# Kernel optimization log

Measured on AMD Instinct MI355X. Metric: run time of the kernel, lower is better.

Reference implementation:

```python
import jax, jax.numpy as jnp
import numpy as np

B_, L, DM = 2, 1024, 1024
DIN = 2048            # expand * d_model
HD = 64               # headdim
NH = DIN // HD        # 32 heads
DS = 64               # d_state
NG = 1                # ngroups
TH = NH * (DS // 2)   # theta dim = 1024
SPLITS = np.cumsum([DIN, DIN, NG * DS, NG * DS, NH, TH]).tolist()
EPS = 1e-5

def _rms(x, w):
    return x * jax.lax.rsqrt(jnp.mean(x * x, -1, keepdims=True) + EPS) * w

def setup_inputs():
    ks = jax.random.split(jax.random.key(0), 8)
    d_in = 2 * DIN + 2 * NG * DS + NH + TH + NH  # 5312
    u = jax.random.normal(ks[0], (B_, L, DM), jnp.float32)
    in_proj_w = jax.random.normal(ks[1], (d_in, DM), jnp.float32) * 0.02
    out_proj_w = jax.random.normal(ks[2], (DM, DIN), jnp.float32) * 0.02
    # dt_bias init as in module: inv-softplus of dt ~ logUniform(dt_min, dt_max)
    dt = jnp.exp(jax.random.uniform(ks[3], (NH,)) * (np.log(0.1) - np.log(0.001)) + np.log(0.001))
    dt_bias = dt + jnp.log(-jnp.expm1(-dt))
    A_log = jnp.log(jax.random.uniform(ks[4], (NH,), minval=1.0, maxval=16.0))
    D = jnp.ones((NH,), jnp.float32)
    B_norm_w = jnp.ones((DS,), jnp.float32)
    C_norm_w = jnp.ones((DS,), jnp.float32)
    B_bias = jnp.ones((NH, DS), jnp.float32)
    C_bias = jnp.ones((NH, DS), jnp.float32)
    norm_w = jnp.ones((DIN,), jnp.float32)
    return dict(u=u, in_proj_w=in_proj_w, dt_bias=dt_bias, A_log=A_log, D=D,
                B_norm_w=B_norm_w, C_norm_w=C_norm_w, B_bias=B_bias, C_bias=C_bias,
                norm_w=norm_w, out_proj_w=out_proj_w)

def reference(u, in_proj_w, dt_bias, A_log, D, B_norm_w, C_norm_w, B_bias, C_bias, norm_w, out_proj_w):
    zxbcdt = u @ in_proj_w.T                                  # (b,l,5312)
    z, x, Br, Cr, dtr, thr, lamr = jnp.split(zxbcdt, SPLITS, axis=-1)
    dt = jax.nn.softplus(dtr + dt_bias)                       # (b,l,h)
    A = -jnp.exp(A_log)                                       # (h,) negative
    x = x.reshape(B_, L, NH, HD)
    # BC norm at group level, then group->head expansion, then head-specific bias
    Bg = _rms(Br.reshape(B_, L, NG, DS), B_norm_w)
    Cg = _rms(Cr.reshape(B_, L, NG, DS), C_norm_w)
    Bh = jnp.broadcast_to(Bg, (B_, L, NH, DS)) + B_bias
    Ch = jnp.broadcast_to(Cg, (B_, L, NH, DS)) + C_bias
    # data-dependent RoPE with cumulative angles
    th_cs = jnp.cumsum(thr.reshape(B_, L, NH, DS // 2), axis=1)
    c, s = jnp.cos(th_cs), jnp.sin(th_cs)
    def rot(v):
        v1, v2 = v[..., :DS // 2], v[..., DS // 2:]
        return jnp.concatenate([v1 * c - v2 * s, v1 * s + v2 * c], -1)
    Bh, Ch = rot(Bh), rot(Ch)
    # trapezoidal discretization coefficients
    lam = jax.nn.sigmoid(lamr)                                # (b,l,h) in [0,1]
    alpha = jnp.exp(dt * A)
    gamma = lam * dt
    beta = (1.0 - lam) * dt * alpha
    def step(carry, inp):
        h, bx_prev = carry
        x_t, B_t, C_t, a_t, b_t, g_t = inp
        bx = x_t[..., :, None] * B_t[..., None, :]            # (b,h,p,n)
        h = a_t[..., None, None] * h + b_t[..., None, None] * bx_prev + g_t[..., None, None] * bx
        y = jnp.einsum('bhn,bhpn->bhp', C_t, h)
        return (h, bx), y
    m = lambda t: jnp.moveaxis(t, 1, 0)                       # seq-major for scan
    h0 = jnp.zeros((B_, NH, HD, DS), u.dtype)
    _, ys = jax.lax.scan(step, (h0, h0), (m(x), m(Bh), m(Ch), m(alpha), m(beta), m(gamma)))
    y = jnp.moveaxis(ys, 0, 1) + x * D[:, None]               # D skip, per head
    y = y.reshape(B_, L, DIN)
    # RMSNormGated, norm_before_gate=False: norm(y * silu(z)) * w
    g = y * jax.nn.silu(z)
    out = _rms(g, norm_w)
    return out @ out_proj_w.T
```

## Files before the change

### kernel.cpp

```cpp
#include <hip/hip_runtime.h>
#include <hip/hip_bf16.h>

#define DMODEL 1024
#define DIN    2048
#define NH     32
#define HD     64
#define DS     64
#define LSEQ   1024
#define BB     2
#define DTOT   5312
#define ROWS   (BB*LSEQ)
#define OFF_Z   0
#define OFF_X   2048
#define OFF_BR  4096
#define OFF_CR  4160
#define OFF_DT  4224
#define OFF_TH  4256
#define OFF_LAM 5280
#define NZX     4096
#define NREM    (DTOT - NZX)
#define NSEG 8
#define SEG  (LSEQ / NSEG)

typedef short  s16x8 __attribute__((ext_vector_type(8)));
typedef float  f32x4 __attribute__((ext_vector_type(4)));
typedef unsigned short u16;

__device__ __forceinline__ unsigned int f2bf(float f) {
    unsigned int u = __float_as_uint(f);
    u += 0x7fffu + ((u >> 16) & 1u);
    return u >> 16;
}
__device__ __forceinline__ unsigned int pk(float x, float y) {
    return f2bf(x) | (f2bf(y) << 16);
}
__device__ __forceinline__ void split1(float v, u16& hi, u16& lo) {
    const unsigned int h = f2bf(v);
    hi = (u16)h;
    lo = (u16)f2bf(v - __uint_as_float(h << 16));
}
__device__ __forceinline__ void split8(const float4 a, const float4 b,
                                       s16x8& hi, s16x8& lo) {
    u16 h_, l_;
    split1(a.x, h_, l_); hi[0] = (short)h_; lo[0] = (short)l_;
    split1(a.y, h_, l_); hi[1] = (short)h_; lo[1] = (short)l_;
    split1(a.z, h_, l_); hi[2] = (short)h_; lo[2] = (short)l_;
    split1(a.w, h_, l_); hi[3] = (short)h_; lo[3] = (short)l_;
    split1(b.x, h_, l_); hi[4] = (short)h_; lo[4] = (short)l_;
    split1(b.y, h_, l_); hi[5] = (short)h_; lo[5] = (short)l_;
    split1(b.z, h_, l_); hi[6] = (short)h_; lo[6] = (short)l_;
    split1(b.w, h_, l_); hi[7] = (short)h_; lo[7] = (short)l_;
}
__device__ __forceinline__ void cvt8(const float4 a, const float4 b, s16x8& hi) {
    hi[0] = (short)f2bf(a.x); hi[1] = (short)f2bf(a.y);
    hi[2] = (short)f2bf(a.z); hi[3] = (short)f2bf(a.w);
    hi[4] = (short)f2bf(b.x); hi[5] = (short)f2bf(b.y);
    hi[6] = (short)f2bf(b.z); hi[7] = (short)f2bf(b.w);
}

typedef const __attribute__((address_space(1))) unsigned int glb_u32;
typedef __attribute__((address_space(3))) unsigned int lds_u32;
__device__ __forceinline__ void gload16(const void* g, void* l) {
    __builtin_amdgcn_global_load_lds((glb_u32*)g, (lds_u32*)l, 16, 0, 0);
}

#define SWZ(row) (((row) >> 1) & 3)

__global__ __launch_bounds__(256) void conv_u(const float* __restrict__ src,
        u16* __restrict__ hi, u16* __restrict__ lo) {
    const size_t i4 = ((size_t)blockIdx.x * 256 + threadIdx.x) * 4;
    const float4 v = *(const float4*)(src + i4);
    const unsigned int h0 = f2bf(v.x), h1 = f2bf(v.y), h2 = f2bf(v.z), h3 = f2bf(v.w);
    uint2 hw, lw;
    hw.x = h0 | (h1 << 16); hw.y = h2 | (h3 << 16);
    lw.x = pk(v.x - __uint_as_float(h0 << 16), v.y - __uint_as_float(h1 << 16));
    lw.y = pk(v.z - __uint_as_float(h2 << 16), v.w - __uint_as_float(h3 << 16));
    *(uint2*)(hi + i4) = hw;
    *(uint2*)(lo + i4) = lw;
}

__global__ __launch_bounds__(256) void conv_w(const float* __restrict__ src,
        u16* __restrict__ hi, u16* __restrict__ lo) {
    const size_t i4 = ((size_t)blockIdx.x * 256 + threadIdx.x) * 4;
    const float4 v = *(const float4*)(src + i4);
    const unsigned int h0 = f2bf(v.x), h1 = f2bf(v.y), h2 = f2bf(v.z), h3 = f2bf(v.w);
    uint2 hw, lw;
    hw.x = h0 | (h1 << 16); hw.y = h2 | (h3 << 16);
    lw.x = pk(v.x - __uint_as_float(h0 << 16), v.y - __uint_as_float(h1 << 16));
    lw.y = pk(v.z - __uint_as_float(h2 << 16), v.w - __uint_as_float(h3 << 16));
    *(uint2*)(hi + i4) = hw;
    if ((i4 >> 10) >= NZX)
        *(uint2*)(lo + (i4 - (size_t)NZX * DMODEL)) = lw;
}

__global__ __launch_bounds__(256) void conv_wo(const float* __restrict__ src,
        u16* __restrict__ hi) {
    const size_t i4 = ((size_t)blockIdx.x * 256 + threadIdx.x) * 4;
    const float4 v = *(const float4*)(src + i4);
    uint2 hw;
    hw.x = pk(v.x, v.y); hw.y = pk(v.z, v.w);
    *(uint2*)(hi + i4) = hw;
}

__global__ __launch_bounds__(256) void mfma_gemm_zx(const u16* __restrict__ uA_,
                                                    const u16* __restrict__ uW,
                                                    float* __restrict__ zx) {
    __shared__ u16 Al[2][128 * 32];
    __shared__ u16 Bl[2][128 * 32];
    const int tid = threadIdx.x;
    const int m0 = blockIdx.y * 128, n0 = blockIdx.x * 128;
    const int lane = tid & 63, wave = tid >> 6;
    const int wr = wave >> 1, wc = wave & 1;
    const int lr = lane >> 4, lc = lane & 15;
    const int sr = tid >> 2;
    const int sc = (((tid & 3) ^ SWZ(tid >> 2)) * 8);

    f32x4 acc[4][4] = {};

    const u16* pA = uA_ + (size_t)(m0 + sr) * DMODEL + sc;
    const u16* pB = uW  + (size_t)(n0 + sr) * DMODEL + sc;

#define STAGE_ZX(buf, k0) {                                              \
        gload16(pA + (k0), &Al[buf][tid * 8]);                           \
        gload16(pA + (k0) + (size_t)64 * DMODEL, &Al[buf][tid * 8 + 2048]); \
        gload16(pB + (k0), &Bl[buf][tid * 8]);                           \
        gload16(pB + (k0) + (size_t)64 * DMODEL, &Bl[buf][tid * 8 + 2048]); }

    STAGE_ZX(0, 0);
    __syncthreads();
    int cur = 0;
    for (int k0 = 0; k0 < DMODEL; k0 += 32) {
        if (k0 + 32 < DMODEL) STAGE_ZX(cur ^ 1, k0 + 32);
        s16x8 af[4], bf[4];
        #pragma unroll
        for (int f = 0; f < 4; ++f) {
            const int ra = wr * 64 + f * 16 + lc;
            af[f] = *(const s16x8*)&Al[cur][ra * 32 + ((lr ^ SWZ(ra)) * 8)];
            const int rb = wc * 64 + f * 16 + lc;
            bf[f] = *(const s16x8*)&Bl[cur][rb * 32 + ((lr ^ SWZ(rb)) * 8)];
        }
        #pragma unroll
        for (int fm = 0; fm < 4; ++fm)
            #pragma unroll
            for (int fn = 0; fn < 4; ++fn)
                acc[fm][fn] = __builtin_amdgcn_mfma_f32_16x16x32_bf16(
                    af[fm], bf[fn], acc[fm][fn], 0, 0, 0);
        __syncthreads();
        cur ^= 1;
    }
#undef STAGE_ZX

    #pragma unroll
    for (int fm = 0; fm < 4; ++fm)
        #pragma unroll
        for (int fn = 0; fn < 4; ++fn) {
            const size_t col = n0 + wc * 64 + fn * 16 + lc;
            #pragma unroll
            for (int j = 0; j < 4; ++j) {
                const size_t row = m0 + wr * 64 + fm * 16 + lr * 4 + j;
                zx[row * DTOT + col] = acc[fm][fn][j];
            }
        }
}

__global__ __launch_bounds__(256) void mfma_gemm_out(const u16* __restrict__ A,
                                                     const u16* __restrict__ B,
                                                     float* __restrict__ C,
                                                     int K, int ldc) {
    __shared__ u16 Als[2][128 * 32];
    __shared__ u16 Bls[2][64 * 32];
    const int tid = threadIdx.x;
    const int m0 = blockIdx.y * 128, n0 = blockIdx.x * 64;
    const int lane = tid & 63, wave = tid >> 6;
    const int wr = wave >> 1, wc = wave & 1;
    const int lr = lane >> 4, lc = lane & 15;
    const int sr = tid >> 2;
    const int sc = (((tid & 3) ^ SWZ(tid >> 2)) * 8);

    f32x4 acc[4][2] = {};

    const u16* pA = A + (size_t)(m0 + sr) * K + sc;
    const u16* pB = B + (size_t)(n0 + sr) * K + sc;

#define STAGE_OUT(buf, k0) {                                             \
        gload16(pA + (k0), &Als[buf][tid * 8]);                          \
        gload16(pA + (k0) + (size_t)64 * K, &Als[buf][tid * 8 + 2048]);  \
        gload16(pB + (k0), &Bls[buf][tid * 8]); }

    STAGE_OUT(0, 0);
    __syncthreads();
    int cur = 0;
    for (int k0 = 0; k0 < K; k0 += 32) {
        if (k0 + 32 < K) STAGE_OUT(cur ^ 1, k0 + 32);
        s16x8 af[4], bf[2];
        #pragma unroll
        for (int f = 0; f < 4; ++f) {
            const int ra = wr * 64 + f * 16 + lc;
            af[f] = *(const s16x8*)&Als[cur][ra * 32 + ((lr ^ SWZ(ra)) * 8)];
        }
        #pragma unroll
        for (int f = 0; f < 2; ++f) {
            const int rb = wc * 32 + f * 16 + lc;
            bf[f] = *(const s16x8*)&Bls[cur][rb * 32 + ((lr ^ SWZ(rb)) * 8)];
        }
        #pragma unroll
        for (int fm = 0; fm < 4; ++fm)
            #pragma unroll
            for (int fn = 0; fn < 2; ++fn)
                acc[fm][fn] = __builtin_amdgcn_mfma_f32_16x16x32_bf16(
                    af[fm], bf[fn], acc[fm][fn], 0, 0, 0);
        __syncthreads();
        cur ^= 1;
    }
#undef STAGE_OUT

    #pragma unroll
    for (int fm = 0; fm < 4; ++fm)
        #pragma unroll
        for (int fn = 0; fn < 2; ++fn) {
            const size_t col = n0 + wc * 32 + fn * 16 + lc;
            #pragma unroll
            for (int j = 0; j < 4; ++j) {
                const size_t row = m0 + wr * 64 + fm * 16 + lr * 4 + j;
                C[row * (size_t)ldc + col] = acc[fm][fn][j];
            }
        }
}

__global__ __launch_bounds__(256) void mfma_gemm_rem3(const u16* __restrict__ uh,
        const u16* __restrict__ ul, const u16* __restrict__ wh,
        const u16* __restrict__ wl, float* __restrict__ zxr) {
    __shared__ u16 Ah[2][128 * 32], Alo[2][128 * 32];
    __shared__ u16 Bh[2][64 * 32],  Blo[2][64 * 32];
    const int tid = threadIdx.x;
    const int m0 = blockIdx.y * 128, n0 = blockIdx.x * 64;
    const int lane = tid & 63, wave = tid >> 6;
    const int wr = wave >> 1, wc = wave & 1;
    const int lr = lane >> 4, lc = lane & 15;
    const int sr = tid >> 2;
    const int sc = (((tid & 3) ^ SWZ(tid >> 2)) * 8);

    f32x4 acc[4][2] = {};

    const u16* pAh = uh + (size_t)(m0 + sr) * DMODEL + sc;
    const u16* pAl = ul + (size_t)(m0 + sr) * DMODEL + sc;
    const u16* pBh = wh + (size_t)(n0 + sr) * DMODEL + sc;
    const u16* pBl = wl + (size_t)(n0 + sr) * DMODEL + sc;

#define STAGE_R3(buf, k0) {                                                  \
        gload16(pAh + (k0), &Ah[buf][tid * 8]);                              \
        gload16(pAh + (k0) + (size_t)64 * DMODEL, &Ah[buf][tid * 8 + 2048]); \
        gload16(pAl + (k0), &Alo[buf][tid * 8]);                             \
        gload16(pAl + (k0) + (size_t)64 * DMODEL, &Alo[buf][tid * 8 + 2048]);\
        gload16(pBh + (k0), &Bh[buf][tid * 8]);                              \
        gload16(pBl + (k0), &Blo[buf][tid * 8]); }

    STAGE_R3(0, 0);
    __syncthreads();
    int cur = 0;
    for (int k0 = 0; k0 < DMODEL; k0 += 32) {
        if (k0 + 32 < DMODEL) STAGE_R3(cur ^ 1, k0 + 32);
        s16x8 ahf[4], alf[4], bhf[2], blf[2];
        #pragma unroll
        for (int f = 0; f < 4; ++f) {
            const int ra = wr * 64 + f * 16 + lc;
            const int oa = ra * 32 + ((lr ^ SWZ(ra)) * 8);
            ahf[f] = *(const s16x8*)&Ah[cur][oa];
            alf[f] = *(const s16x8*)&Alo[cur][oa];
        }
        #pragma unroll
        for (int f = 0; f < 2; ++f) {
            const int rb = wc * 32 + f * 16 + lc;
            const int ob = rb * 32 + ((lr ^ SWZ(rb)) * 8);
            bhf[f] = *(const s16x8*)&Bh[cur][ob];
            blf[f] = *(const s16x8*)&Blo[cur][ob];
        }
        #pragma unroll
        for (int fm = 0; fm < 4; ++fm)
            #pragma unroll
            for (int fn = 0; fn < 2; ++fn) {
                acc[fm][fn] = __builtin_amdgcn_mfma_f32_16x16x32_bf16(
                    ahf[fm], bhf[fn], acc[fm][fn], 0, 0, 0);
                acc[fm][fn] = __builtin_amdgcn_mfma_f32_16x16x32_bf16(
                    ahf[fm], blf[fn], acc[fm][fn], 0, 0, 0);
                acc[fm][fn] = __builtin_amdgcn_mfma_f32_16x16x32_bf16(
                    alf[fm], bhf[fn], acc[fm][fn], 0, 0, 0);
            }
        __syncthreads();
        cur ^= 1;
    }
#undef STAGE_R3

    #pragma unroll
    for (int fm = 0; fm < 4; ++fm)
        #pragma unroll
        for (int fn = 0; fn < 2; ++fn) {
            const size_t col = n0 + wc * 32 + fn * 16 + lc;
            #pragma unroll
            for (int j = 0; j < 4; ++j) {
                const size_t row = m0 + wr * 64 + fm * 16 + lr * 4 + j;
                zxr[row * DTOT + col] = acc[fm][fn][j];
            }
        }
}

__global__ __launch_bounds__(64) void prep_kernel(const float* __restrict__ zx,
        const float* __restrict__ dt_bias, const float* __restrict__ A_log,
        const float* __restrict__ B_norm_w, const float* __restrict__ C_norm_w,
        float* __restrict__ Bg, float* __restrict__ Cg,
        float4* __restrict__ abg4) {
    const int bl = blockIdx.x;
    const int b = bl >> 10, l = bl & (LSEQ - 1);
    const int t  = threadIdx.x;
    const float* row = zx + (size_t)bl * DTOT;
    const float br = row[OFF_BR + t];
    const float cr = row[OFF_CR + t];
    float ssb = br * br, ssc = cr * cr;
    #pragma unroll
    for (int k = 1; k < 64; k <<= 1) { ssb += __shfl_xor(ssb, k); ssc += __shfl_xor(ssc, k); }
    const float scB = rsqrtf(ssb * (1.f / 64.f) + 1e-5f);
    const float scC = rsqrtf(ssc * (1.f / 64.f) + 1e-5f);
    Bg[(size_t)bl * 64 + t] = br * scB * B_norm_w[t];
    Cg[(size_t)bl * 64 + t] = cr * scC * C_norm_w[t];
    if (t < NH) {
        const float dtr = row[OFF_DT + t] + dt_bias[t];
        const float dt  = (dtr > 20.f) ? dtr : log1pf(expf(dtr));
        const float lamr = row[OFF_LAM + t];
        const float lam  = 1.f / (1.f + expf(-lamr));
        const float Ah   = -expf(A_log[t]);
        const float al   = expf(dt * Ah);
        const float bp   = (1.f - lam) * dt;
        const size_t o = ((size_t)b * NH + t) * LSEQ + l;
        abg4[o] = make_float4(al, bp * al, lam * dt, bp);
    }
}

__global__ __launch_bounds__(256) void cumsum_kernel(const float* __restrict__ zx,
                                                     float* __restrict__ th_cs) {
    const int bh = blockIdx.x;
    const int b = bh >> 5, h = bh & 31;
    const int d = threadIdx.x & 31, seg = threadIdx.x >> 5;
    const float* base = zx + (size_t)b * LSEQ * DTOT + OFF_TH + h * 32 + d;
    float* out = th_cs + (size_t)b * LSEQ * 1024 + h * 32 + d;
    __shared__ float sums[8][33];
    const int l0 = seg * 128;
    float s = 0.f;
    #pragma unroll 4
    for (int i = 0; i < 128; ++i) s += base[(size_t)(l0 + i) * DTOT];
    sums[seg][d] = s;
    __syncthreads();
    float acc = 0.f;
    for (int s2 = 0; s2 < seg; ++s2) acc += sums[s2][d];
    #pragma unroll 4
    for (int i = 0; i < 128; ++i) {
        acc += base[(size_t)(l0 + i) * DTOT];
        out[(size_t)(l0 + i) * 1024] = acc;
    }
}

__global__ __launch_bounds__(256) void rot_kernel(const float* __restrict__ th_cs,
        const float* __restrict__ Bg, const float* __restrict__ Cg,
        const float* __restrict__ B_bias, const float* __restrict__ C_bias,
        float* __restrict__ Brot, float* __restrict__ Crot) {
    const size_t idx = (size_t)blockIdx.x * 256 + threadIdx.x;
    const int j = (int)(idx & 31);
    const int h = (int)((idx >> 5) & 31);
    const size_t bl = idx >> 10;
    const int l = (int)(bl & (LSEQ - 1));
    const int b = (int)(bl >> 10);
    const float th = th_cs[idx];
    float s, c;
    sincosf(th, &s, &c);
    float v1 = Bg[bl * 64 + j]      + B_bias[h * 64 + j];
    float v2 = Bg[bl * 64 + 32 + j] + B_bias[h * 64 + 32 + j];
    const size_t ob = ((size_t)(b * NH + h) * LSEQ + l) * DS + j;
    Brot[ob]      = v1 * c - v2 * s;
    Brot[ob + 32] = v1 * s + v2 * c;
    v1 = Cg[bl * 64 + j]      + C_bias[h * 64 + j];
    v2 = Cg[bl * 64 + 32 + j] + C_bias[h * 64 + 32 + j];
    Crot[ob]      = v1 * c - v2 * s;
    Crot[ob + 32] = v1 * s + v2 * c;
}

__global__ __launch_bounds__(64) void wcalc_kernel(const float4* __restrict__ abg4,
        float* __restrict__ wbuf, float* __restrict__ aprod,
        float* __restrict__ bscale, float* __restrict__ Lbuf) {
    const int bh = blockIdx.x;
    const int lane = threadIdx.x;
    const int seg = lane >> 3, sub = lane & 7;
    const int t0 = seg * SEG;
    const int sbase = t0 + sub * 16;
    const float4* ab = abg4 + (size_t)bh * LSEQ;

    float part = 0.f;
    #pragma unroll
    for (int i = 0; i < 16; ++i) part += logf(ab[sbase + i].x);
    float incl = part;
    #pragma unroll
    for (int d = 1; d < 8; d <<= 1) {
        const float v = __shfl_up(incl, d, 8);
        if (sub >= d) incl += v;
    }
    const float LE = __shfl(incl, 7, 8);
    float Lrun = incl - part;

    for (int i = 0; i < 16; ++i) {
        const int s = sbase + i;
        const float4 A = ab[s];
        Lrun += logf(A.x);
        Lbuf[(size_t)bh * LSEQ + s] = Lrun;
        float w;
        if ((s & (SEG - 1)) == (SEG - 1)) w = A.z;
        else w = __expf(LE - Lrun) * (A.z + ab[s + 1].w);
        wbuf[(size_t)bh * LSEQ + s] = w;
    }
    if (sub == 0) {
        aprod[bh * NSEG + seg] = __expf(LE);
        bscale[bh * NSEG + seg] = (seg > 0) ? __expf(LE) * ab[t0].w : 0.f;
    }
}

#define WK 136
__global__ __launch_bounds__(256) void hseg_gemm(const float* __restrict__ zx,
        const float* __restrict__ Brot, const float* __restrict__ wbuf,
        float* __restrict__ hseg) {
    __shared__ u16 XH[64][WK], XL[64][WK], BHs[64][WK], BLs[64][WK];
    const int blk = blockIdx.x;
    const int seg = blk & (NSEG - 1), bh = blk >> 3;
    const int b = bh >> 5, h = bh & 31;
    const int tid = threadIdx.x;

    {
        const int sIdx = tid >> 1, half = tid & 1;
        const int t = seg * SEG + sIdx;
        const float wv = wbuf[(size_t)bh * LSEQ + t];
        const float* xsrc = zx + ((size_t)b * LSEQ + t) * DTOT + OFF_X + h * 64 + half * 32;
        const float* bsrc = Brot + ((size_t)bh * LSEQ + t) * DS + half * 32;
        #pragma unroll
        for (int i = 0; i < 32; i += 4) {
            const float4 xv = *(const float4*)(xsrc + i);
            const float4 bv = *(const float4*)(bsrc + i);
            const int p0 = half * 32 + i;
            u16 hi, lo;
            split1(xv.x * wv, hi, lo); XH[p0 + 0][sIdx] = hi; XL[p0 + 0][sIdx] = lo;
            split1(xv.y * wv, hi, lo); XH[p0 + 1][sIdx] = hi; XL[p0 + 1][sIdx] = lo;
            split1(xv.z * wv, hi, lo); XH[p0 + 2][sIdx] = hi; XL[p0 + 2][sIdx] = lo;
            split1(xv.w * wv, hi, lo); XH[p0 + 3][sIdx] = hi; XL[p0 + 3][sIdx] = lo;
            split1(bv.x, hi, lo); BHs[p0 + 0][sIdx] = hi; BLs[p0 + 0][sIdx] = lo;
            split1(bv.y, hi, lo); BHs[p0 + 1][sIdx] = hi; BLs[p0 + 1][sIdx] = lo;
            split1(bv.z, hi, lo); BHs[p0 + 2][sIdx] = hi; BLs[p0 + 2][sIdx] = lo;
            split1(bv.w, hi, lo); BHs[p0 + 3][sIdx] = hi; BLs[p0 + 3][sIdx] = lo;
        }
    }
    __syncthreads();

    const int lane = tid & 63, wave = tid >> 6;
    const int wR = wave >> 1, wC = wave & 1;
    const int lr = lane >> 4, lc = lane & 15;

    f32x4 acc[2][2] = {};
    #pragma unroll
    for (int ks = 0; ks < 4; ++ks) {
        const int k0 = ks * 32;
        s16x8 xh[2], xl[2], bhf[2], blf[2];
        #pragma unroll
        for (int f = 0; f < 2; ++f) {
            const int pr = wR * 32 + f * 16 + lc;
            xh[f] = *(const s16x8*)&XH[pr][k0 + lr * 8];
            xl[f] = *(const s16x8*)&XL[pr][k0 + lr * 8];
            const int nr = wC * 32 + f * 16 + lc;
            bhf[f] = *(const s16x8*)&BHs[nr][k0 + lr * 8];
            blf[f] = *(const s16x8*)&BLs[nr][k0 + lr * 8];
        }
        #pragma unroll
        for (int fm = 0; fm < 2; ++fm)
            #pragma unroll
            for (int fn = 0; fn < 2; ++fn) {
                acc[fm][fn] = __builtin_amdgcn_mfma_f32_16x16x32_bf16(
                    xh[fm], bhf[fn], acc[fm][fn], 0, 0, 0);
                acc[fm][fn] = __builtin_amdgcn_mfma_f32_16x16x32_bf16(
                    xh[fm], blf[fn], acc[fm][fn], 0, 0, 0);
                acc[fm][fn] = __builtin_amdgcn_mfma_f32_16x16x32_bf16(
                    xl[fm], bhf[fn], acc[fm][fn], 0, 0, 0);
            }
    }

    float* hp = hseg + ((size_t)(bh * NSEG + seg) * HD) * DS;
    #pragma unroll
    for (int fm = 0; fm < 2; ++fm)
        #pragma unroll
        for (int fn = 0; fn < 2; ++fn) {
            const int n = wC * 32 + fn * 16 + lc;
            #pragma unroll
            for (int j = 0; j < 4; ++j) {
                const int p = wR * 32 + fm * 16 + lr * 4 + j;
                hp[p * DS + n] = acc[fm][fn][j];
            }
        }
}

__global__ __launch_bounds__(256) void scan_fix(float* __restrict__ hseg,
        const float* __restrict__ aprod, const float* __restrict__ bscale,
        const float* __restrict__ zx, const float* __restrict__ Brot,
        const float4* __restrict__ abg4) {
    const int blk = blockIdx.x;
    const int ptile = blk & 3, h = (blk >> 2) & 31, b = blk >> 7;
    const int tid = threadIdx.x;
    const int pl = tid >> 4, ng = tid & 15;
    const int p = ptile * 16 + pl;
    const int n0 = ng * 4;
    const size_t bh = (size_t)b * NH + h;

    float4 cur = make_float4(0.f, 0.f, 0.f, 0.f);
    #pragma unroll
    for (int s = 0; s < NSEG; ++s) {
        float* hp = hseg + (((bh * NSEG + s) * HD + p) * DS + n0);
        float4 tmp = *(const float4*)hp;
        float4 hst = cur;
        if (s > 0) {
            const float bs = bscale[bh * NSEG + s];
            const float bp0 = abg4[bh * LSEQ + s * SEG].w;
            const int tm1 = s * SEG - 1;
            const float4 Bm = *(const float4*)(Brot + ((size_t)bh * LSEQ + tm1) * DS + n0);
            const float xm = zx[((size_t)b * LSEQ + tm1) * DTOT + OFF_X + h * HD + p];
            const float fb = bs * xm;
            const float f1 = bp0 * xm;
            tmp.x = fmaf(fb, Bm.x, tmp.x);
            tmp.y = fmaf(fb, Bm.y, tmp.y);
            tmp.z = fmaf(fb, Bm.z, tmp.z);
            tmp.w = fmaf(fb, Bm.w, tmp.w);
            hst.x = fmaf(f1, Bm.x, hst.x);
            hst.y = fmaf(f1, Bm.y, hst.y);
            hst.z = fmaf(f1, Bm.z, hst.z);
            hst.w = fmaf(f1, Bm.w, hst.w);
        }
        *(float4*)hp = hst;
        const float a = aprod[bh * NSEG + s];
        cur.x = fmaf(a, cur.x, tmp.x);
        cur.y = fmaf(a, cur.y, tmp.y);
        cur.z = fmaf(a, cur.z, tmp.z);
        cur.w = fmaf(a, cur.w, tmp.w);
    }
}

#define GWF 132
#define XTS 72
__global__ __launch_bounds__(256, 2) void ssd_y(const float* __restrict__ zx,
        const float* __restrict__ Brot, const float* __restrict__ Crot,
        const float4* __restrict__ abg4, const float* __restrict__ hseg,
        const float* __restrict__ Lbuf, const float* __restrict__ Dp,
        float* __restrict__ yb) {
    __shared__ float Gw[128 * GWF];
    __shared__ u16 XTh[64 * XTS];
    __shared__ float Ls[128], gbs[128], gms[128], eLs[128];

    const int blk = blockIdx.x;
    const int seg = blk & (NSEG - 1), bh = blk >> 3;
    const int b = bh >> 5, h = bh & 31;
    const int tid = threadIdx.x;
    const int t0 = seg * SEG;
    const int lane = tid & 63, wave = tid >> 6;
    const int wr = wave >> 1, wc = wave & 1;
    const int lr = lane >> 4, lc = lane & 15;

    if (tid < 128) {
        const int t = t0 + tid;
        const float4 A = abg4[(size_t)bh * LSEQ + t];
        const float Lv = Lbuf[(size_t)bh * LSEQ + t];
        Ls[tid] = Lv;
        gms[tid] = A.z;
        gbs[tid] = (tid < 127) ? A.z + abg4[(size_t)bh * LSEQ + t + 1].w : 0.f;
        eLs[tid] = __expf(Lv);
    }
    __syncthreads();

    const float* Cbase = Crot + ((size_t)bh * LSEQ + t0) * DS;
    const float* Bbase = Brot + ((size_t)bh * LSEQ + t0) * DS;
    const float* Hbase = hseg + ((size_t)(bh * NSEG + seg) * HD) * DS;
    const float* Xbase = zx + ((size_t)b * LSEQ + t0) * DTOT + OFF_X + h * 64;

    f32x4 accP[4][2] = {};
    f32x4 accG[4][4] = {};
    #pragma unroll
    for (int ks = 0; ks < 2; ++ks) {
        const int k0 = ks * 32 + lr * 8;
        s16x8 ch[4], cl4[4], bh4[4], bl4[4], hh2[2];
        #pragma unroll
        for (int f = 0; f < 4; ++f) {
            const int rowc = wr * 64 + f * 16 + lc;
            const float4 c0 = *(const float4*)(Cbase + (size_t)rowc * DS + k0);
            const float4 c1 = *(const float4*)(Cbase + (size_t)rowc * DS + k0 + 4);
            split8(c0, c1, ch[f], cl4[f]);
            const int rowb = wc * 64 + f * 16 + lc;
            const float4 b0 = *(const float4*)(Bbase + (size_t)rowb * DS + k0);
            const float4 b1 = *(const float4*)(Bbase + (size_t)rowb * DS + k0 + 4);
            split8(b0, b1, bh4[f], bl4[f]);
        }
        #pragma unroll
        for (int f = 0; f < 2; ++f) {
            const int rowp = wc * 32 + f * 16 + lc;
            const float4 h0 = *(const float4*)(Hbase + (size_t)rowp * DS + k0);
            const float4 h1 = *(const float4*)(Hbase + (size_t)rowp * DS + k0 + 4);
            cvt8(h0, h1, hh2[f]);
        }
        #pragma unroll
        for (int fm = 0; fm < 4; ++fm) {
            #pragma unroll
            for (int fn = 0; fn < 4; ++fn) {
                accG[fm][fn] = __builtin_amdgcn_mfma_f32_16x16x32_bf16(
                    ch[fm], bh4[fn], accG[fm][fn], 0, 0, 0);
                accG[fm][fn] = __builtin_amdgcn_mfma_f32_16x16x32_bf16(
                    ch[fm], bl4[fn], accG[fm][fn], 0, 0, 0);
                accG[fm][fn] = __builtin_amdgcn_mfma_f32_16x16x32_bf16(
                    cl4[fm], bh4[fn], accG[fm][fn], 0, 0, 0);
            }
            #pragma unroll
            for (int fn = 0; fn < 2; ++fn) {
                accP[fm][fn] = __builtin_amdgcn_mfma_f32_16x16x32_bf16(
                    ch[fm], hh2[fn], accP[fm][fn], 0, 0, 0);
                accP[fm][fn] = __builtin_amdgcn_mfma_f32_16x16x32_bf16(
                    cl4[fm], hh2[fn], accP[fm][fn], 0, 0, 0);
            }
        }
    }

    const float Dh = Dp[h];
    #pragma unroll
    for (int fm = 0; fm < 4; ++fm)
        #pragma unroll
        for (int fn = 0; fn < 4; ++fn)
            #pragma unroll
            for (int jj = 0; jj < 4; ++jj) {
                const int i = wr * 64 + fm * 16 + lr * 4 + jj;
                const int j = wc * 64 + fn * 16 + lc;
                float v;
                if (j < i)       v = accG[fm][fn][jj] * __expf(Ls[i] - Ls[j]) * gbs[j];
                else if (j == i) v = accG[fm][fn][jj] * gms[i] + Dh;
                else             v = 0.f;
                Gw[i * GWF + j] = v;
            }

    f32x4 accY[4][2];
    #pragma unroll
    for (int fm = 0; fm < 4; ++fm)
        #pragma unroll
        for (int fn = 0; fn < 2; ++fn)
            #pragma unroll
            for (int jj = 0; jj < 4; ++jj) {
                const int i = wr * 64 + fm * 16 + lr * 4 + jj;
                accY[fm][fn][jj] = eLs[i] * accP[fm][fn][jj];
            }

#define STAGE_XT(H) {                                                        \
        const int lp = tid >> 2, pq = (tid & 3) * 16;                        \
        const float* xs = Xbase + (size_t)((H) * 64 + lp) * DTOT + pq;       \
        _Pragma("unroll")                                                    \
        for (int i = 0; i < 16; i += 4) {                                    \
            const float4 xv = *(const float4*)(xs + i);                      \
            XTh[(pq + i + 0) * XTS + lp] = (u16)f2bf(xv.x);                  \
            XTh[(pq + i + 1) * XTS + lp] = (u16)f2bf(xv.y);                  \
            XTh[(pq + i + 2) * XTS + lp] = (u16)f2bf(xv.z);                  \
            XTh[(pq + i + 3) * XTS + lp] = (u16)f2bf(xv.w);                  \
        }                                                                    \
    }
    STAGE_XT(0);
    __syncthreads();

    #pragma unroll
    for (int ks = 0; ks < 4; ++ks) {
        if (ks == 2) {
            __syncthreads();
            STAGE_XT(1);
            __syncthreads();
        }
        const int k0 = ks * 32 + lr * 8;
        const int kl = (ks & 1) * 32 + lr * 8;
        s16x8 gh4[4], gl4[4], xf[2];
        #pragma unroll
        for (int f = 0; f < 4; ++f) {
            const int rowi = wr * 64 + f * 16 + lc;
            const float4 g0 = *(const float4*)&Gw[rowi * GWF + k0];
            const float4 g1 = *(const float4*)&Gw[rowi * GWF + k0 + 4];
            split8(g0, g1, gh4[f], gl4[f]);
        }
        #pragma unroll
        for (int f = 0; f < 2; ++f) {
            const int rowp = wc * 32 + f * 16 + lc;
            xf[f] = *(const s16x8*)&XTh[rowp * XTS + kl];
        }
        #pragma unroll
        for (int fm = 0; fm < 4; ++fm)
            #pragma unroll
            for (int fn = 0; fn < 2; ++fn) {
                accY[fm][fn] = __builtin_amdgcn_mfma_f32_16x16x32_bf16(
                    gh4[fm], xf[fn], accY[fm][fn], 0, 0, 0);
                accY[fm][fn] = __builtin_amdgcn_mfma_f32_16x16x32_bf16(
                    gl4[fm], xf[fn], accY[fm][fn], 0, 0, 0);
            }
    }
#undef STAGE_XT

    #pragma unroll
    for (int fm = 0; fm < 4; ++fm)
        #pragma unroll
        for (int fn = 0; fn < 2; ++fn) {
            const int p = wc * 32 + fn * 16 + lc;
            #pragma unroll
            for (int jj = 0; jj < 4; ++jj) {
                const int i = wr * 64 + fm * 16 + lr * 4 + jj;
                yb[((size_t)b * LSEQ + t0 + i) * DIN + h * 64 + p] = accY[fm][fn][jj];
            }
        }
}

__global__ __launch_bounds__(256) void gate_norm_kernel(const float* __restrict__ yb,
        const float* __restrict__ zx, const float* __restrict__ norm_w,
        u16* __restrict__ gnb) {
    const int bl = blockIdx.x;
    const int tid = threadIdx.x;
    const float* yrow = yb + (size_t)bl * DIN;
    const float* zrow = zx + (size_t)bl * DTOT + OFF_Z;
    float g[8];
    float ss = 0.f;
    #pragma unroll
    for (int i = 0; i < 8; ++i) {
        const int c = tid + i * 256;
        const float yv = yrow[c];
        const float zv = zrow[c];
        const float sg = 1.f / (1.f + expf(-zv));
        const float gv = yv * zv * sg;
        g[i] = gv;
        ss += gv * gv;
    }
    #pragma unroll
    for (int k = 1; k < 64; k <<= 1) ss += __shfl_xor(ss, k);
    __shared__ float wsum[4];
    if ((tid & 63) == 0) wsum[tid >> 6] = ss;
    __syncthreads();
    ss = wsum[0] + wsum[1] + wsum[2] + wsum[3];
    const float sc = rsqrtf(ss * (1.f / 2048.f) + 1e-5f);
    #pragma unroll
    for (int i = 0; i < 8; ++i) {
        const int c = tid + i * 256;
        gnb[(size_t)bl * DIN + c] = (u16)f2bf(g[i] * sc * norm_w[c]);
    }
}

extern "C" void kernel_launch(void* const* d_in, const int* in_sizes, int n_in,
                              void* d_out, int out_size, void* d_ws, size_t ws_size,
                              hipStream_t stream) {
    const float* u          = (const float*)d_in[0];
    const float* in_proj_w  = (const float*)d_in[1];
    const float* dt_bias    = (const float*)d_in[2];
    const float* A_log      = (const float*)d_in[3];
    const float* Dp         = (const float*)d_in[4];
    const float* B_norm_w   = (const float*)d_in[5];
    const float* C_norm_w   = (const float*)d_in[6];
    const float* B_bias     = (const float*)d_in[7];
    const float* C_bias     = (const float*)d_in[8];
    const float* norm_w     = (const float*)d_in[9];
    const float* out_proj_w = (const float*)d_in[10];
    float* out = (float*)d_out;

    float* p = (float*)d_ws;
    float* zx    = p; p += (size_t)ROWS * DTOT;
    float* th_cs = p; p += (size_t)ROWS * 1024;
    float* Brot  = p; p += (size_t)ROWS * 2048;
    float* Crot  = p; p += (size_t)ROWS * 2048;
    float* Bg    = p; p += (size_t)ROWS * 64;
    float* Cg    = p; p += (size_t)ROWS * 64;
    float4* abg4 = (float4*)p; p += (size_t)ROWS * NH * 4;
    float* yb    = p; p += (size_t)ROWS * 2048;
    float* hseg   = th_cs;
    float* aprod  = Bg;
    float* bscale = Bg + 512;
    float* Lbuf   = Bg + 2048;
    float* wbuf   = Cg;

    u16* u_bf = (u16*)Brot;
    u16* u_lo = u_bf + (size_t)ROWS * DMODEL;
    u16* w_bf = u_lo + (size_t)ROWS * DMODEL;
    u16* w_lo = w_bf + (size_t)DTOT * DMODEL;
    u16* gn_bf = (u16*)Brot;
    u16* wo_bf = gn_bf + (size_t)ROWS * DIN;

    conv_u<<<(ROWS * DMODEL / 4) / 256, 256, 0, stream>>>(u, u_bf, u_lo);
    conv_w<<<((size_t)DTOT * DMODEL / 4) / 256, 256, 0, stream>>>(in_proj_w, w_bf, w_lo);
    mfma_gemm_zx<<<dim3(NZX / 128, ROWS / 128), 256, 0, stream>>>(u_bf, w_bf, zx);
    mfma_gemm_rem3<<<dim3(NREM / 64, ROWS / 128), 256, 0, stream>>>(
        u_bf, u_lo, w_bf + (size_t)NZX * DMODEL, w_lo, zx + NZX);
    prep_kernel<<<ROWS, 64, 0, stream>>>(zx, dt_bias, A_log, B_norm_w, C_norm_w,
                                         Bg, Cg, abg4);
    cumsum_kernel<<<BB * NH, 256, 0, stream>>>(zx, th_cs);
    rot_kernel<<<(ROWS * 1024) / 256, 256, 0, stream>>>(th_cs, Bg, Cg, B_bias, C_bias,
                                                        Brot, Crot);
    wcalc_kernel<<<BB * NH, 64, 0, stream>>>(abg4, wbuf, aprod, bscale, Lbuf);
    hseg_gemm<<<BB * NH * NSEG, 256, 0, stream>>>(zx, Brot, wbuf, hseg);
    scan_fix<<<BB * NH * 4, 256, 0, stream>>>(hseg, aprod, bscale, zx, Brot, abg4);
    ssd_y<<<BB * NH * NSEG, 256, 0, stream>>>(zx, Brot, Crot, abg4, hseg, Lbuf, Dp, yb);
    conv_wo<<<(DMODEL * DIN / 4) / 256, 256, 0, stream>>>(out_proj_w, wo_bf);
    gate_norm_kernel<<<ROWS, 256, 0, stream>>>(yb, zx, norm_w, gn_bf);
    mfma_gemm_out<<<dim3(DMODEL / 64, ROWS / 128), 256, 0, stream>>>(
        gn_bf, wo_bf, out, DIN, DMODEL);
}
```

Before: 197.1 us.

## Double GEMM K-tile to 64 and merge conversion kernels into fewer launches

The zx and out-projection GEMMs now stage 64-wide K tiles with an 8-way XOR swizzle and run two MFMA sub-steps per tile, which halves the number of barriers and loop iterations. The u/w bf16 conversion kernels are merged into one launch, and the out_proj weight conversion is merged into the gate-norm kernel, removing two launches. The cost is double the LDS per block (64KB for zx), which may reduce occupancy.

```diff
diff --git a/kernel.cpp b/kernel.cpp
--- a/kernel.cpp
+++ b/kernel.cpp
@@ -64,87 +64,89 @@
     __builtin_amdgcn_global_load_lds((glb_u32*)g, (lds_u32*)l, 16, 0, 0);
 }
 
-#define SWZ(row) (((row) >> 1) & 3)
-
-__global__ __launch_bounds__(256) void conv_u(const float* __restrict__ src,
-        u16* __restrict__ hi, u16* __restrict__ lo) {
-    const size_t i4 = ((size_t)blockIdx.x * 256 + threadIdx.x) * 4;
-    const float4 v = *(const float4*)(src + i4);
-    const unsigned int h0 = f2bf(v.x), h1 = f2bf(v.y), h2 = f2bf(v.z), h3 = f2bf(v.w);
-    uint2 hw, lw;
-    hw.x = h0 | (h1 << 16); hw.y = h2 | (h3 << 16);
-    lw.x = pk(v.x - __uint_as_float(h0 << 16), v.y - __uint_as_float(h1 << 16));
-    lw.y = pk(v.z - __uint_as_float(h2 << 16), v.w - __uint_as_float(h3 << 16));
-    *(uint2*)(hi + i4) = hw;
-    *(uint2*)(lo + i4) = lw;
-}
-
-__global__ __launch_bounds__(256) void conv_w(const float* __restrict__ src,
-        u16* __restrict__ hi, u16* __restrict__ lo) {
-    const size_t i4 = ((size_t)blockIdx.x * 256 + threadIdx.x) * 4;
-    const float4 v = *(const float4*)(src + i4);
-    const unsigned int h0 = f2bf(v.x), h1 = f2bf(v.y), h2 = f2bf(v.z), h3 = f2bf(v.w);
-    uint2 hw, lw;
-    hw.x = h0 | (h1 << 16); hw.y = h2 | (h3 << 16);
-    lw.x = pk(v.x - __uint_as_float(h0 << 16), v.y - __uint_as_float(h1 << 16));
-    lw.y = pk(v.z - __uint_as_float(h2 << 16), v.w - __uint_as_float(h3 << 16));
-    *(uint2*)(hi + i4) = hw;
-    if ((i4 >> 10) >= NZX)
-        *(uint2*)(lo + (i4 - (size_t)NZX * DMODEL)) = lw;
-}
-
-__global__ __launch_bounds__(256) void conv_wo(const float* __restrict__ src,
-        u16* __restrict__ hi) {
-    const size_t i4 = ((size_t)blockIdx.x * 256 + threadIdx.x) * 4;
-    const float4 v = *(const float4*)(src + i4);
-    uint2 hw;
-    hw.x = pk(v.x, v.y); hw.y = pk(v.z, v.w);
-    *(uint2*)(hi + i4) = hw;
+#define SWZ(row)  (((row) >> 1) & 3)
+#define SWZ8(row) (((row) >> 1) & 7)
+
+#define CONV_U_BLOCKS (ROWS * DMODEL / 4 / 256)
+#define CONV_W_BLOCKS ((DTOT * DMODEL / 4) / 256)
+__global__ __launch_bounds__(256) void conv_uw(const float* __restrict__ usrc,
+        const float* __restrict__ wsrc, u16* __restrict__ u_hi,
+        u16* __restrict__ u_lo, u16* __restrict__ w_hi, u16* __restrict__ w_lo) {
+    const int bid = blockIdx.x;
+    if (bid < CONV_U_BLOCKS) {
+        const size_t i4 = ((size_t)bid * 256 + threadIdx.x) * 4;
+        const float4 v = *(const float4*)(usrc + i4);
+        const unsigned int h0 = f2bf(v.x), h1 = f2bf(v.y), h2 = f2bf(v.z), h3 = f2bf(v.w);
+        uint2 hw, lw;
+        hw.x = h0 | (h1 << 16); hw.y = h2 | (h3 << 16);
+        lw.x = pk(v.x - __uint_as_float(h0 << 16), v.y - __uint_as_float(h1 << 16));
+        lw.y = pk(v.z - __uint_as_float(h2 << 16), v.w - __uint_as_float(h3 << 16));
+        *(uint2*)(u_hi + i4) = hw;
+        *(uint2*)(u_lo + i4) = lw;
+    } else {
+        const size_t i4 = ((size_t)(bid - CONV_U_BLOCKS) * 256 + threadIdx.x) * 4;
+        const float4 v = *(const float4*)(wsrc + i4);
+        const unsigned int h0 = f2bf(v.x), h1 = f2bf(v.y), h2 = f2bf(v.z), h3 = f2bf(v.w);
+        uint2 hw, lw;
+        hw.x = h0 | (h1 << 16); hw.y = h2 | (h3 << 16);
+        lw.x = pk(v.x - __uint_as_float(h0 << 16), v.y - __uint_as_float(h1 << 16));
+        lw.y = pk(v.z - __uint_as_float(h2 << 16), v.w - __uint_as_float(h3 << 16));
+        *(uint2*)(w_hi + i4) = hw;
+        if ((i4 >> 10) >= NZX)
+            *(uint2*)(w_lo + (i4 - (size_t)NZX * DMODEL)) = lw;
+    }
 }
 
 __global__ __launch_bounds__(256) void mfma_gemm_zx(const u16* __restrict__ uA_,
                                                     const u16* __restrict__ uW,
                                                     float* __restrict__ zx) {
-    __shared__ u16 Al[2][128 * 32];
-    __shared__ u16 Bl[2][128 * 32];
+    __shared__ u16 Al[2][128 * 64];
+    __shared__ u16 Bl[2][128 * 64];
     const int tid = threadIdx.x;
     const int m0 = blockIdx.y * 128, n0 = blockIdx.x * 128;
     const int lane = tid & 63, wave = tid >> 6;
     const int wr = wave >> 1, wc = wave & 1;
     const int lr = lane >> 4, lc = lane & 15;
-    const int sr = tid >> 2;
-    const int sc = (((tid & 3) ^ SWZ(tid >> 2)) * 8);
+    const int sr = tid >> 3;
+    const int sc = (((tid & 7) ^ ((tid >> 4) & 7)) * 8);
 
     f32x4 acc[4][4] = {};
 
     const u16* pA = uA_ + (size_t)(m0 + sr) * DMODEL + sc;
     const u16* pB = uW  + (size_t)(n0 + sr) * DMODEL + sc;
 
-#define STAGE_ZX(buf, k0) {                                              \
-        gload16(pA + (k0), &Al[buf][tid * 8]);                           \
-        gload16(pA + (k0) + (size_t)64 * DMODEL, &Al[buf][tid * 8 + 2048]); \
-        gload16(pB + (k0), &Bl[buf][tid * 8]);                           \
-        gload16(pB + (k0) + (size_t)64 * DMODEL, &Bl[buf][tid * 8 + 2048]); }
+#define STAGE_ZX(buf, k0) {                                                   \
+        gload16(pA + (k0),                        &Al[buf][tid * 8]);         \
+        gload16(pA + (k0) + (size_t)32 * DMODEL,  &Al[buf][tid * 8 + 2048]);  \
+        gload16(pA + (k0) + (size_t)64 * DMODEL,  &Al[buf][tid * 8 + 4096]);  \
+        gload16(pA + (k0) + (size_t)96 * DMODEL,  &Al[buf][tid * 8 + 6144]);  \
+        gload16(pB + (k0),                        &Bl[buf][tid * 8]);         \
+        gload16(pB + (k0) + (size_t)32 * DMODEL,  &Bl[buf][tid * 8 + 2048]);  \
+        gload16(pB + (k0) + (size_t)64 * DMODEL,  &Bl[buf][tid * 8 + 4096]);  \
+        gload16(pB + (k0) + (size_t)96 * DMODEL,  &Bl[buf][tid * 8 + 6144]); }
 
     STAGE_ZX(0, 0);
     __syncthreads();
     int cur = 0;
-    for (int k0 = 0; k0 < DMODEL; k0 += 32) {
-        if (k0 + 32 < DMODEL) STAGE_ZX(cur ^ 1, k0 + 32);
-        s16x8 af[4], bf[4];
-        #pragma unroll
-        for (int f = 0; f < 4; ++f) {
-            const int ra = wr * 64 + f * 16 + lc;
-            af[f] = *(const s16x8*)&Al[cur][ra * 32 + ((lr ^ SWZ(ra)) * 8)];
-            const int rb = wc * 64 + f * 16 + lc;
-            bf[f] = *(const s16x8*)&Bl[cur][rb * 32 + ((lr ^ SWZ(rb)) * 8)];
-        }
-        #pragma unroll
-        for (int fm = 0; fm < 4; ++fm)
-            #pragma unroll
-            for (int fn = 0; fn < 4; ++fn)
-                acc[fm][fn] = __builtin_amdgcn_mfma_f32_16x16x32_bf16(
-                    af[fm], bf[fn], acc[fm][fn], 0, 0, 0);
+    for (int k0 = 0; k0 < DMODEL; k0 += 64) {
+        if (k0 + 64 < DMODEL) STAGE_ZX(cur ^ 1, k0 + 64);
+        #pragma unroll
+        for (int kk = 0; kk < 2; ++kk) {
+            s16x8 af[4], bf[4];
+            #pragma unroll
+            for (int f = 0; f < 4; ++f) {
+                const int ra = wr * 64 + f * 16 + lc;
+                af[f] = *(const s16x8*)&Al[cur][ra * 64 + (((kk * 4 + lr) ^ SWZ8(ra)) * 8)];
+                const int rb = wc * 64 + f * 16 + lc;
+                bf[f] = *(const s16x8*)&Bl[cur][rb * 64 + (((kk * 4 + lr) ^ SWZ8(rb)) * 8)];
+            }
+            #pragma unroll
+            for (int fm = 0; fm < 4; ++fm)
+                #pragma unroll
+                for (int fn = 0; fn < 4; ++fn)
+                    acc[fm][fn] = __builtin_amdgcn_mfma_f32_16x16x32_bf16(
+                        af[fm], bf[fn], acc[fm][fn], 0, 0, 0);
+        }
         __syncthreads();
         cur ^= 1;
     }
@@ -167,48 +169,54 @@
                                                      const u16* __restrict__ B,
                                                      float* __restrict__ C,
                                                      int K, int ldc) {
-    __shared__ u16 Als[2][128 * 32];
-    __shared__ u16 Bls[2][64 * 32];
+    __shared__ u16 Als[2][128 * 64];
+    __shared__ u16 Bls[2][64 * 64];
     const int tid = threadIdx.x;
     const int m0 = blockIdx.y * 128, n0 = blockIdx.x * 64;
     const int lane = tid & 63, wave = tid >> 6;
     const int wr = wave >> 1, wc = wave & 1;
     const int lr = lane >> 4, lc = lane & 15;
-    const int sr = tid >> 2;
-    const int sc = (((tid & 3) ^ SWZ(tid >> 2)) * 8);
+    const int sr = tid >> 3;
+    const int sc = (((tid & 7) ^ ((tid >> 4) & 7)) * 8);
 
     f32x4 acc[4][2] = {};
 
     const u16* pA = A + (size_t)(m0 + sr) * K + sc;
     const u16* pB = B + (size_t)(n0 + sr) * K + sc;
 
-#define STAGE_OUT(buf, k0) {                                             \
-        gload16(pA + (k0), &Als[buf][tid * 8]);                          \
-        gload16(pA + (k0) + (size_t)64 * K, &Als[buf][tid * 8 + 2048]);  \
-        gload16(pB + (k0), &Bls[buf][tid * 8]); }
+#define STAGE_OUT(buf, k0) {                                                  \
+        gload16(pA + (k0),                   &Als[buf][tid * 8]);             \
+        gload16(pA + (k0) + (size_t)32 * K,  &Als[buf][tid * 8 + 2048]);      \
+        gload16(pA + (k0) + (size_t)64 * K,  &Als[buf][tid * 8 + 4096]);      \
+        gload16(pA + (k0) + (size_t)96 * K,  &Als[buf][tid * 8 + 6144]);      \
+        gload16(pB + (k0),                   &Bls[buf][tid * 8]);             \
+        gload16(pB + (k0) + (size_t)32 * K,  &Bls[buf][tid * 8 + 2048]); }
 
     STAGE_OUT(0, 0);
     __syncthreads();
     int cur = 0;
-    for (int k0 = 0; k0 < K; k0 += 32) {
-        if (k0 + 32 < K) STAGE_OUT(cur ^ 1, k0 + 32);
-        s16x8 af[4], bf[2];
-        #pragma unroll
-        for (int f = 0; f < 4; ++f) {
-            const int ra = wr * 64 + f * 16 + lc;
-            af[f] = *(const s16x8*)&Als[cur][ra * 32 + ((lr ^ SWZ(ra)) * 8)];
-        }
-        #pragma unroll
-        for (int f = 0; f < 2; ++f) {
-            const int rb = wc * 32 + f * 16 + lc;
-            bf[f] = *(const s16x8*)&Bls[cur][rb * 32 + ((lr ^ SWZ(rb)) * 8)];
-        }
-        #pragma unroll
-        for (int fm = 0; fm < 4; ++fm)
-            #pragma unroll
-            for (int fn = 0; fn < 2; ++fn)
-                acc[fm][fn] = __builtin_amdgcn_mfma_f32_16x16x32_bf16(
-                    af[fm], bf[fn], acc[fm][fn], 0, 0, 0);
+    for (int k0 = 0; k0 < K; k0 += 64) {
+        if (k0 + 64 < K) STAGE_OUT(cur ^ 1, k0 + 64);
+        #pragma unroll
+        for (int kk = 0; kk < 2; ++kk) {
+            s16x8 af[4], bf[2];
+            #pragma unroll
+            for (int f = 0; f < 4; ++f) {
+                const int ra = wr * 64 + f * 16 + lc;
+                af[f] = *(const s16x8*)&Als[cur][ra * 64 + (((kk * 4 + lr) ^ SWZ8(ra)) * 8)];
+            }
+            #pragma unroll
+            for (int f = 0; f < 2; ++f) {
+                const int rb = wc * 32 + f * 16 + lc;
+                bf[f] = *(const s16x8*)&Bls[cur][rb * 64 + (((kk * 4 + lr) ^ SWZ8(rb)) * 8)];
+            }
+            #pragma unroll
+            for (int fm = 0; fm < 4; ++fm)
+                #pragma unroll
+                for (int fn = 0; fn < 2; ++fn)
+                    acc[fm][fn] = __builtin_amdgcn_mfma_f32_16x16x32_bf16(
+                        af[fm], bf[fn], acc[fm][fn], 0, 0, 0);
+        }
         __syncthreads();
         cur ^= 1;
     }
@@ -713,36 +721,45 @@
         }
 }
 
-__global__ __launch_bounds__(256) void gate_norm_kernel(const float* __restrict__ yb,
+__global__ __launch_bounds__(256) void gate_convwo(const float* __restrict__ yb,
         const float* __restrict__ zx, const float* __restrict__ norm_w,
-        u16* __restrict__ gnb) {
-    const int bl = blockIdx.x;
-    const int tid = threadIdx.x;
-    const float* yrow = yb + (size_t)bl * DIN;
-    const float* zrow = zx + (size_t)bl * DTOT + OFF_Z;
-    float g[8];
-    float ss = 0.f;
-    #pragma unroll
-    for (int i = 0; i < 8; ++i) {
-        const int c = tid + i * 256;
-        const float yv = yrow[c];
-        const float zv = zrow[c];
-        const float sg = 1.f / (1.f + expf(-zv));
-        const float gv = yv * zv * sg;
-        g[i] = gv;
-        ss += gv * gv;
-    }
-    #pragma unroll
-    for (int k = 1; k < 64; k <<= 1) ss += __shfl_xor(ss, k);
-    __shared__ float wsum[4];
-    if ((tid & 63) == 0) wsum[tid >> 6] = ss;
-    __syncthreads();
-    ss = wsum[0] + wsum[1] + wsum[2] + wsum[3];
-    const float sc = rsqrtf(ss * (1.f / 2048.f) + 1e-5f);
-    #pragma unroll
-    for (int i = 0; i < 8; ++i) {
-        const int c = tid + i * 256;
-        gnb[(size_t)bl * DIN + c] = (u16)f2bf(g[i] * sc * norm_w[c]);
+        u16* __restrict__ gnb, const float* __restrict__ wo_src,
+        u16* __restrict__ wo_hi) {
+    if (blockIdx.x < ROWS) {
+        const int bl = blockIdx.x;
+        const int tid = threadIdx.x;
+        const float* yrow = yb + (size_t)bl * DIN;
+        const float* zrow = zx + (size_t)bl * DTOT + OFF_Z;
+        float g[8];
+        float ss = 0.f;
+        #pragma unroll
+        for (int i = 0; i < 8; ++i) {
+            const int c = tid + i * 256;
+            const float yv = yrow[c];
+            const float zv = zrow[c];
+            const float sg = 1.f / (1.f + expf(-zv));
+            const float gv = yv * zv * sg;
+            g[i] = gv;
+            ss += gv * gv;
+        }
+        #pragma unroll
+        for (int k = 1; k < 64; k <<= 1) ss += __shfl_xor(ss, k);
+        __shared__ float wsum[4];
+        if ((tid & 63) == 0) wsum[tid >> 6] = ss;
+        __syncthreads();
+        ss = wsum[0] + wsum[1] + wsum[2] + wsum[3];
+        const float sc = rsqrtf(ss * (1.f / 2048.f) + 1e-5f);
+        #pragma unroll
+        for (int i = 0; i < 8; ++i) {
+            const int c = tid + i * 256;
+            gnb[(size_t)bl * DIN + c] = (u16)f2bf(g[i] * sc * norm_w[c]);
+        }
+    } else {
+        const size_t i4 = ((size_t)(blockIdx.x - ROWS) * 256 + threadIdx.x) * 4;
+        const float4 v = *(const float4*)(wo_src + i4);
+        uint2 hw;
+        hw.x = pk(v.x, v.y); hw.y = pk(v.z, v.w);
+        *(uint2*)(wo_hi + i4) = hw;
     }
 }
 
@@ -784,8 +801,8 @@
     u16* gn_bf = (u16*)Brot;
     u16* wo_bf = gn_bf + (size_t)ROWS * DIN;
 
-    conv_u<<<(ROWS * DMODEL / 4) / 256, 256, 0, stream>>>(u, u_bf, u_lo);
-    conv_w<<<((size_t)DTOT * DMODEL / 4) / 256, 256, 0, stream>>>(in_proj_w, w_bf, w_lo);
+    conv_uw<<<CONV_U_BLOCKS + CONV_W_BLOCKS, 256, 0, stream>>>(
+        u, in_proj_w, u_bf, u_lo, w_bf, w_lo);
     mfma_gemm_zx<<<dim3(NZX / 128, ROWS / 128), 256, 0, stream>>>(u_bf, w_bf, zx);
     mfma_gemm_rem3<<<dim3(NREM / 64, ROWS / 128), 256, 0, stream>>>(
         u_bf, u_lo, w_bf + (size_t)NZX * DMODEL, w_lo, zx + NZX);
@@ -798,8 +815,8 @@
     hseg_gemm<<<BB * NH * NSEG, 256, 0, stream>>>(zx, Brot, wbuf, hseg);
     scan_fix<<<BB * NH * 4, 256, 0, stream>>>(hseg, aprod, bscale, zx, Brot, abg4);
     ssd_y<<<BB * NH * NSEG, 256, 0, stream>>>(zx, Brot, Crot, abg4, hseg, Lbuf, Dp, yb);
-    conv_wo<<<(DMODEL * DIN / 4) / 256, 256, 0, stream>>>(out_proj_w, wo_bf);
-    gate_norm_kernel<<<ROWS, 256, 0, stream>>>(yb, zx, norm_w, gn_bf);
+    gate_convwo<<<ROWS + (DMODEL * DIN / 4) / 256, 256, 0, stream>>>(
+        yb, zx, norm_w, gn_bf, out_proj_w, wo_bf);
     mfma_gemm_out<<<dim3(DMODEL / 64, ROWS / 128), 256, 0, stream>>>(
         gn_bf, wo_bf, out, DIN, DMODEL);
 }
```

Result: faster. 187.1 us (-5.1%).
